# Kernel optimization log

Measured on AMD Instinct MI355X. Metric: run time of the kernel, lower is better.

## Reference

```python
import jax, jax.numpy as jnp
from jax import lax
import numpy as np

B, C, H, W = 4, 128, 160, 160
C2 = 2 * C          # dwconv / channel-attention width
FP_HID = 2 * C      # Feature_Pool ratio=2
CA_HID = C2 // 16   # Channel_Attention ratio=16


def setup_inputs() -> dict:
    key = jax.random.key(0)
    ks = jax.random.split(key, 20)
    s = lambda *sh: 0.02
    return {
        "RGB": jax.random.normal(ks[0], (B, C, H, W), jnp.float32),
        "T": jax.random.normal(ks[1], (B, C, H, W), jnp.float32),
        # Feature_Pool (shared module applied to both RGB and T)
        "fp_down_w": jax.random.normal(ks[2], (FP_HID, C), jnp.float32) * 0.02,
        "fp_down_b": jnp.zeros((FP_HID,), jnp.float32),
        "fp_up_w": jax.random.normal(ks[3], (C, FP_HID), jnp.float32) * 0.02,
        "fp_up_b": jnp.zeros((C,), jnp.float32),
        # dwconv: Conv2d(2c, 2c, k=7, pad=3, groups=c) -> weight [2c, 2, 7, 7]
        "dw_w": jax.random.normal(ks[4], (C2, 2, 7, 7), jnp.float32) * 0.02,
        "dw_b": jnp.zeros((C2,), jnp.float32),
        # Channel_Attention on 2c
        "ca_down_w": jax.random.normal(ks[5], (CA_HID, C2), jnp.float32) * 0.02,
        "ca_down_b": jnp.zeros((CA_HID,), jnp.float32),
        "ca_up_w": jax.random.normal(ks[6], (C2, CA_HID), jnp.float32) * 0.02,
        "ca_up_b": jnp.zeros((C2,), jnp.float32),
        # Spatial_Attention 1x1 convs (c -> 1), stored as [c] vectors + scalar bias
        "sr_w": jax.random.normal(ks[7], (C,), jnp.float32) * 0.02,
        "sr_b": jnp.zeros((1,), jnp.float32),
        "st_w": jax.random.normal(ks[8], (C,), jnp.float32) * 0.02,
        "st_b": jnp.zeros((1,), jnp.float32),
    }


def _feature_pool(x, dw, db, uw, ub):
    # AdaptiveAvgPool2d(1) -> Linear -> GELU(exact) -> Linear ; returns [b, c]
    y = jnp.mean(x, axis=(2, 3))
    y = jax.nn.gelu(y @ dw.T + db, approximate=False)
    return y @ uw.T + ub


def _channel_att(x, dw, db, uw, ub):
    # AdaptiveMaxPool2d(1) -> Linear -> GELU(exact) -> Linear ; returns [b, 2c, 1, 1]
    y = jnp.max(x, axis=(2, 3))
    y = jax.nn.gelu(y @ dw.T + db, approximate=False)
    y = y @ uw.T + ub
    return y[:, :, None, None]


def reference(RGB, T, fp_down_w, fp_down_b, fp_up_w, fp_up_b, dw_w, dw_b,
              ca_down_w, ca_down_b, ca_up_w, ca_up_b, sr_w, sr_b, st_w, st_b):
    b, c, h, w = RGB.shape
    rgb_y = _feature_pool(RGB, fp_down_w, fp_down_b, fp_up_w, fp_up_b)
    t_y = _feature_pool(T, fp_down_w, fp_down_b, fp_up_w, fp_up_b)
    rgb_y = rgb_y / jnp.linalg.norm(rgb_y, axis=1, keepdims=True)
    t_y = t_y / jnp.linalg.norm(t_y, axis=1, keepdims=True)
    # logits_per = c * rgb_y[b,c,1] @ t_y[b,1,c] -> [b, c, c]
    logits = c * rgb_y[:, :, None] * t_y[:, None, :]
    # Faithful to torch.diagonal default (dim1=0, dim2=1): result[j,k] = logits[k,k,j],
    # shape [c, min(b,c)] = [c, b]; then reshape to (b, c, 1, 1). Requires b <= c.
    diag = jnp.diagonal(logits, axis1=0, axis2=1)
    cross_gate = jax.nn.sigmoid(diag).reshape(b, c, 1, 1)
    add_gate = 1.0 - cross_gate

    New_RGB_e = RGB * cross_gate
    New_T_e = T * cross_gate
    New_RGB_c = RGB * add_gate
    New_T_c = T * add_gate

    x_cat_e = jnp.concatenate([New_RGB_e, New_T_e], axis=1)  # [b, 2c, h, w]
    dw_out = lax.conv_general_dilated(
        x_cat_e, dw_w, window_strides=(1, 1), padding=[(3, 3), (3, 3)],
        dimension_numbers=("NCHW", "OIHW", "NCHW"), feature_group_count=c,
    ) + dw_b[None, :, None, None]

    fuse_gate = jax.nn.sigmoid(_channel_att(dw_out, ca_down_w, ca_down_b, ca_up_w, ca_up_b))
    rgb_gate_e, t_gate_e = fuse_gate[:, :c], fuse_gate[:, c:]

    New_RGB = New_RGB_e * rgb_gate_e + New_RGB_c
    New_T = New_T_e * t_gate_e + New_T_c

    # 1x1 conv c->1 (with bias) for each stream
    f_r = jnp.einsum("bchw,c->bhw", New_RGB, sr_w)[:, None] + sr_b[0]  # [b,1,h,w]
    f_t = jnp.einsum("bchw,c->bhw", New_T, st_w)[:, None] + st_b[0]
    att = jax.nn.softmax(jnp.concatenate([f_r, f_t], axis=1), axis=1)  # [b,2,h,w]

    New_RGB = New_RGB * att[:, 0:1]
    New_T = New_T * att[:, 1:2]
    return New_RGB, New_T
```

## Files before the change

kernel.cpp:

```cpp
#include <hip/hip_runtime.h>
#include <cfloat>
#include <cmath>

#define HW 25600
#define WIDTH 160
#define NB 4
#define NC 128

typedef float f32x2 __attribute__((ext_vector_type(2)));
typedef _Float16 h2 __attribute__((ext_vector_type(2)));

__device__ __forceinline__ float gelu_exact(float x) {
    return 0.5f * x * (1.f + erff(x * 0.70710678118654752f));
}
__device__ __forceinline__ float sigmoidf_(float x) {
    return 1.f / (1.f + expf(-x));
}

__device__ __forceinline__ unsigned pack_pkrtz(float a, float b) {
    return __builtin_bit_cast(unsigned, __builtin_amdgcn_cvt_pkrtz(a, b));
}
__device__ __forceinline__ h2 u2h(unsigned u) {
    return __builtin_bit_cast(h2, u);
}
__device__ __forceinline__ float h2sum(h2 h) {
    return (float)h[0] + (float)h[1];
}
__device__ __forceinline__ h2 fma2h(h2 a, h2 b, h2 c) {
    return __builtin_elementwise_fma(a, b, c);
}

__global__ __launch_bounds__(256) void mean_pack_kernel(const float* __restrict__ RGB,
                                                        const float* __restrict__ T,
                                                        const float* __restrict__ dww,
                                                        float* __restrict__ means,
                                                        unsigned* __restrict__ wpk) {
    int p = blockIdx.x;
    if (p >= 1024) {
        int i = (p - 1024) * 256 + threadIdx.x;
        if (i < 128 * 98) {
            int g = i / 98; int r = i - g * 98;
            int ky = r / 14; int r2 = r - ky * 14;
            int oc = r2 / 7; int kx = r2 - oc * 7;
            int o = 2 * g + oc;
            float wa = dww[(o * 2 + 0) * 49 + ky * 7 + kx];
            float wb = dww[(o * 2 + 1) * 49 + ky * 7 + kx];
            wpk[i] = pack_pkrtz(wa, wb);
        }
        return;
    }
    const float* src = (p < 512) ? (RGB + (size_t)p * HW)
                                 : (T + (size_t)(p - 512) * HW);
    const float4* s4 = (const float4*)src;
    float s = 0.f;
    for (int i = threadIdx.x; i < HW / 4; i += 256) {
        float4 v = s4[i];
        s += (v.x + v.y) + (v.z + v.w);
    }
    for (int off = 32; off; off >>= 1) s += __shfl_down(s, off);
    __shared__ float r[4];
    if ((threadIdx.x & 63) == 0) r[threadIdx.x >> 6] = s;
    __syncthreads();
    if (threadIdx.x == 0) means[p] = (r[0] + r[1] + r[2] + r[3]) * (1.f / (float)HW);
}

__global__ __launch_bounds__(256) void mlp_kernel(const float* __restrict__ means,
                                                  const float* __restrict__ dww,
                                                  const float* __restrict__ dwb,
                                                  const float* __restrict__ uww,
                                                  const float* __restrict__ uwb,
                                                  float* __restrict__ ynorm) {
    int tb = blockIdx.x;
    int t = threadIdx.x;
    __shared__ float sm[128];
    __shared__ float sh[256];
    __shared__ float zz[256];
    __shared__ float r4[4];
    if (t < 128) sm[t] = means[tb * 128 + t];
    __syncthreads();
    float a = dwb[t];
    const float* wrow = dww + t * 128;
    for (int c = 0; c < 128; ++c) a += wrow[c] * sm[c];
    sh[t] = gelu_exact(a);
    __syncthreads();
    int c = t & 127, half = t >> 7;
    float z = 0.f;
    const float* urow = uww + c * 256 + half * 128;
    const float* hh = sh + half * 128;
    for (int j = 0; j < 128; ++j) z += urow[j] * hh[j];
    zz[t] = z;
    __syncthreads();
    float y = 0.f;
    if (t < 128) y = zz[t] + zz[t + 128] + uwb[t];
    float p = y * y;
    for (int off = 32; off; off >>= 1) p += __shfl_down(p, off);
    if ((t & 63) == 0) r4[t >> 6] = p;
    __syncthreads();
    float nrm = sqrtf(r4[0] + r4[1] + r4[2] + r4[3]);
    if (t < 128) ynorm[tb * 128 + t] = y / nrm;
}

#define TW2 166
#define THR 22
#define NYT 10
__global__ __launch_bounds__(256, 4) void conv_max_kernel(const float* __restrict__ RGB,
                                                          const float* __restrict__ T,
                                                          const unsigned* __restrict__ wpk,
                                                          const float* __restrict__ ynorm,
                                                          float* __restrict__ part) {
    int orig = blockIdx.x;
    int wg = (orig & 7) * 640 + (orig >> 3);
    int b  = wg / 1280;
    int rr = wg - b * 1280;
    int g  = rr / NYT;
    int yt = rr - g * NYT;
    int t  = threadIdx.x;
    __shared__ unsigned tile[THR * TW2];
    __shared__ float r0s[4], r1s[4];
    int ic0 = 2 * g;
    int c0 = ic0 & 127, c1 = (ic0 + 1) & 127;
    const float* base = (ic0 < 128) ? RGB : T;
    const float* plane0 = base + ((size_t)(b * 128 + c0)) * HW;
    const float* plane1 = base + ((size_t)(b * 128 + c1)) * HW;
    int i0 = b * 128 + c0, i1 = b * 128 + c1;
    int j0 = i0 & 3, k0 = i0 >> 2, j1 = i1 & 3, k1 = i1 >> 2;
    float gate0 = sigmoidf_(128.f * ynorm[j0 * 128 + j0] * ynorm[512 + j0 * 128 + k0]);
    float gate1 = sigmoidf_(128.f * ynorm[j1 * 128 + j1] * ynorm[512 + j1 * 128 + k1]);
    int y0 = yt * 16 - 3;
    for (int e = t; e < THR * TW2; e += 256) {
        int row = e / TW2;
        int col = e - row * TW2;
        int gy = y0 + row, gx = col - 3;
        float v0 = 0.f, v1 = 0.f;
        if (gy >= 0 && gy < 160 && gx >= 0 && gx < 160) {
            int off = gy * WIDTH + gx;
            v0 = plane0[off] * gate0;
            v1 = plane1[off] * gate1;
        }
        tile[e] = pack_pkrtz(v0, v1);
    }
    __syncthreads();
    int xs = (t & 15) * 10;
    int ys = t >> 4;
    h2 zz = (h2)0;
    h2 A0 = zz, A1 = zz, A2 = zz, A3 = zz, A4 = zz;
    h2 A5 = zz, A6 = zz, A7 = zz, A8 = zz, A9 = zz;
    h2 B0 = zz, B1 = zz, B2 = zz, B3 = zz, B4 = zz;
    h2 B5 = zz, B6 = zz, B7 = zz, B8 = zz, B9 = zz;
    const unsigned* wgp = wpk + g * 98;
    #pragma unroll
    for (int ky = 0; ky < 7; ++ky) {
        unsigned wk[14];
        #pragma unroll
        for (int j = 0; j < 14; ++j) wk[j] = wgp[ky * 14 + j];
        const uint2* tr2 = (const uint2*)(tile + (ys + ky) * TW2 + xs);
        unsigned win[16];
        #pragma unroll
        for (int j = 0; j < 8; ++j) {
            uint2 p = tr2[j];
            win[2 * j] = p.x;
            win[2 * j + 1] = p.y;
        }
        #pragma unroll
        for (int kx = 0; kx < 7; ++kx) {
            h2 w0 = u2h(wk[kx]);
            h2 w1 = u2h(wk[7 + kx]);
            h2 v;
            v = u2h(win[kx + 0]); A0 = fma2h(w0, v, A0); B0 = fma2h(w1, v, B0);
            v = u2h(win[kx + 1]); A1 = fma2h(w0, v, A1); B1 = fma2h(w1, v, B1);
            v = u2h(win[kx + 2]); A2 = fma2h(w0, v, A2); B2 = fma2h(w1, v, B2);
            v = u2h(win[kx + 3]); A3 = fma2h(w0, v, A3); B3 = fma2h(w1, v, B3);
            v = u2h(win[kx + 4]); A4 = fma2h(w0, v, A4); B4 = fma2h(w1, v, B4);
            v = u2h(win[kx + 5]); A5 = fma2h(w0, v, A5); B5 = fma2h(w1, v, B5);
            v = u2h(win[kx + 6]); A6 = fma2h(w0, v, A6); B6 = fma2h(w1, v, B6);
            v = u2h(win[kx + 7]); A7 = fma2h(w0, v, A7); B7 = fma2h(w1, v, B7);
            v = u2h(win[kx + 8]); A8 = fma2h(w0, v, A8); B8 = fma2h(w1, v, B8);
            v = u2h(win[kx + 9]); A9 = fma2h(w0, v, A9); B9 = fma2h(w1, v, B9);
        }
    }
    float m0 = fmaxf(fmaxf(fmaxf(h2sum(A0), h2sum(A1)), fmaxf(h2sum(A2), h2sum(A3))),
                     fmaxf(fmaxf(h2sum(A4), h2sum(A5)),
                           fmaxf(fmaxf(h2sum(A6), h2sum(A7)), fmaxf(h2sum(A8), h2sum(A9)))));
    float m1 = fmaxf(fmaxf(fmaxf(h2sum(B0), h2sum(B1)), fmaxf(h2sum(B2), h2sum(B3))),
                     fmaxf(fmaxf(h2sum(B4), h2sum(B5)),
                           fmaxf(fmaxf(h2sum(B6), h2sum(B7)), fmaxf(h2sum(B8), h2sum(B9)))));
    for (int off = 32; off; off >>= 1) {
        m0 = fmaxf(m0, __shfl_down(m0, off));
        m1 = fmaxf(m1, __shfl_down(m1, off));
    }
    if ((t & 63) == 0) { r0s[t >> 6] = m0; r1s[t >> 6] = m1; }
    __syncthreads();
    if (t == 0) {
        m0 = fmaxf(fmaxf(r0s[0], r0s[1]), fmaxf(r0s[2], r0s[3]));
        m1 = fmaxf(fmaxf(r1s[0], r1s[1]), fmaxf(r1s[2], r1s[3]));
        int bb = ((b * 128 + g) * NYT + yt) * 2;
        part[bb] = m0;
        part[bb + 1] = m1;
    }
}

__global__ __launch_bounds__(256) void att_kernel(const float* __restrict__ ynorm,
                                                  const float* __restrict__ part,
                                                  const float* __restrict__ dwb,
                                                  const float* __restrict__ cdw,
                                                  const float* __restrict__ cdb,
                                                  const float* __restrict__ cuw,
                                                  const float* __restrict__ cub,
                                                  const float* __restrict__ srw,
                                                  const float* __restrict__ stw,
                                                  float* __restrict__ coefs) {
    int t = threadIdx.x;
    __shared__ float scg[512];
    __shared__ float smax[1024];
    __shared__ float sh2[64];
    __shared__ float sfg[1024];
    for (int idx = t; idx < 512; idx += 256) {
        int kk = idx >> 2, j = idx & 3;
        scg[idx] = sigmoidf_(128.f * ynorm[j * 128 + j] * ynorm[512 + j * 128 + kk]);
    }
    for (int idx = t; idx < 1024; idx += 256) {
        int b = idx >> 8, o = idx & 255;
        int gg = o >> 1, oc = o & 1;
        const float* pp = part + ((b * 128 + gg) * NYT) * 2 + oc;
        float m = pp[0];
        #pragma unroll
        for (int yt = 1; yt < NYT; ++yt) m = fmaxf(m, pp[yt * 2]);
        smax[idx] = m + dwb[o];
    }
    __syncthreads();
    if (t < 64) {
        int b = t >> 4, j = t & 15;
        float a = cdb[j];
        const float* wrow = cdw + j * 256;
        const float* mx = smax + b * 256;
        for (int o = 0; o < 256; ++o) a += wrow[o] * mx[o];
        sh2[t] = gelu_exact(a);
    }
    __syncthreads();
    for (int idx = t; idx < 1024; idx += 256) {
        int b = idx >> 8, o = idx & 255;
        float z = cub[o];
        const float* ur = cuw + o * 16;
        const float* hh = sh2 + b * 16;
        #pragma unroll
        for (int j = 0; j < 16; ++j) z += ur[j] * hh[j];
        sfg[idx] = sigmoidf_(z);
    }
    __syncthreads();
    for (int idx = t; idx < 512; idx += 256) {
        int b = idx >> 7, c = idx & 127;
        float cgv = scg[idx];
        float ar = cgv * sfg[b * 256 + c] + 1.f - cgv;
        float at = cgv * sfg[b * 256 + 128 + c] + 1.f - cgv;
        coefs[idx] = ar;
        coefs[512 + idx] = at;
        coefs[1024 + idx] = ar * srw[c];
        coefs[1536 + idx] = at * stw[c];
    }
}

__global__ __launch_bounds__(512, 4) void fuse_kernel(const float* __restrict__ RGB,
                                                      const float* __restrict__ T,
                                                      const float* __restrict__ coefs,
                                                      const float* __restrict__ srb,
                                                      const float* __restrict__ stb,
                                                      float* __restrict__ out) {
    int b = blockIdx.y;
    int t = threadIdx.x;
    int w = t >> 6, lane = t & 63;
    int pix = blockIdx.x * 128 + lane * 2;
    __shared__ float sco[4][128];
    if (t < 512) {
        int a = t >> 7, c = t & 127;
        sco[a][c] = coefs[a * 512 + b * 128 + c];
    }
    __syncthreads();
    const float* rp = RGB + (size_t)b * NC * HW;
    const float* tp = T + (size_t)b * NC * HW;
    f32x2 rv[16], tv[16];
    f32x2 df; df.x = 0.f; df.y = 0.f;
    #pragma unroll
    for (int ci = 0; ci < 16; ++ci) {
        int c = w * 16 + ci;
        size_t off = (size_t)c * HW + pix;
        rv[ci] = *(const f32x2*)(rp + off);
        tv[ci] = *(const f32x2*)(tp + off);
        float wrc = sco[2][c], wtc = sco[3][c];
        df.x += rv[ci].x * wrc - tv[ci].x * wtc;
        df.y += rv[ci].y * wrc - tv[ci].y * wtc;
    }
    __shared__ f32x2 sdf[8][64];
    sdf[w][lane] = df;
    __syncthreads();
    float sx = srb[0] - stb[0], sy = sx;
    #pragma unroll
    for (int ww = 0; ww < 8; ++ww) {
        f32x2 d = sdf[ww][lane];
        sx += d.x;
        sy += d.y;
    }
    float ax = sigmoidf_(sx), ay = sigmoidf_(sy);
    float* outR = out + (size_t)b * NC * HW;
    float* outT = out + (size_t)NB * NC * HW + (size_t)b * NC * HW;
    #pragma unroll
    for (int ci = 0; ci < 16; ++ci) {
        int c = w * 16 + ci;
        size_t off = (size_t)c * HW + pix;
        float arc = sco[0][c], atc = sco[1][c];
        f32x2 o1, o2;
        o1.x = rv[ci].x * arc * ax;         o1.y = rv[ci].y * arc * ay;
        o2.x = tv[ci].x * atc * (1.f - ax); o2.y = tv[ci].y * atc * (1.f - ay);
        __builtin_nontemporal_store(o1, (f32x2*)(outR + off));
        __builtin_nontemporal_store(o2, (f32x2*)(outT + off));
    }
}

extern "C" void kernel_launch(void* const* d_in, const int* in_sizes, int n_in,
                              void* d_out, int out_size, void* d_ws, size_t ws_size,
                              hipStream_t stream) {
    const float* RGB       = (const float*)d_in[0];
    const float* T         = (const float*)d_in[1];
    const float* fp_down_w = (const float*)d_in[2];
    const float* fp_down_b = (const float*)d_in[3];
    const float* fp_up_w   = (const float*)d_in[4];
    const float* fp_up_b   = (const float*)d_in[5];
    const float* dw_w      = (const float*)d_in[6];
    const float* dw_b      = (const float*)d_in[7];
    const float* ca_down_w = (const float*)d_in[8];
    const float* ca_down_b = (const float*)d_in[9];
    const float* ca_up_w   = (const float*)d_in[10];
    const float* ca_up_b   = (const float*)d_in[11];
    const float* sr_w      = (const float*)d_in[12];
    const float* sr_b      = (const float*)d_in[13];
    const float* st_w      = (const float*)d_in[14];
    const float* st_b      = (const float*)d_in[15];
    float* out = (float*)d_out;
    float* ws  = (float*)d_ws;

    unsigned* wpk = (unsigned*)(ws + 14336);
    mean_pack_kernel<<<1073, 256, 0, stream>>>(RGB, T, dw_w, ws, wpk);
    mlp_kernel<<<8, 256, 0, stream>>>(ws, fp_down_w, fp_down_b, fp_up_w, fp_up_b, ws + 1024);
    conv_max_kernel<<<5120, 256, 0, stream>>>(RGB, T, wpk, ws + 1024, ws + 2048);
    att_kernel<<<1, 256, 0, stream>>>(ws + 1024, ws + 2048, dw_b, ca_down_w, ca_down_b,
                                      ca_up_w, ca_up_b, sr_w, st_w, ws + 12288);
    fuse_kernel<<<dim3(200, 4), 512, 0, stream>>>(RGB, T, ws + 12288, sr_b, st_b, out);
}
```

Measured before the change: 134.0 us.

## Fuse channel-attention MLP into fuse kernel and simplify tile-load indexing

Removes the single-block att_kernel launch and has every fuse block redundantly compute the channel-attention MLP and gate coefficients for its batch, with the down-projection split across 256 threads. This eliminates one launch, its serial tail, and the coefs round-trip through global memory. The cost is 800 blocks each redoing the small reduction over part and the MLP before streaming. The conv tile loader also replaces per-element division with incremental row/col stepping and unsigned bounds checks.

```diff
diff --git a/kernel.cpp b/kernel.cpp
--- a/kernel.cpp
+++ b/kernel.cpp
@@ -127,26 +127,31 @@
     float gate0 = sigmoidf_(128.f * ynorm[j0 * 128 + j0] * ynorm[512 + j0 * 128 + k0]);
     float gate1 = sigmoidf_(128.f * ynorm[j1 * 128 + j1] * ynorm[512 + j1 * 128 + k1]);
     int y0 = yt * 16 - 3;
-    for (int e = t; e < THR * TW2; e += 256) {
-        int row = e / TW2;
-        int col = e - row * TW2;
-        int gy = y0 + row, gx = col - 3;
-        float v0 = 0.f, v1 = 0.f;
-        if (gy >= 0 && gy < 160 && gx >= 0 && gx < 160) {
-            int off = gy * WIDTH + gx;
-            v0 = plane0[off] * gate0;
-            v1 = plane1[off] * gate1;
+    {
+        int row = t / TW2;
+        int col = t - row * TW2;
+        for (int e = t; e < THR * TW2; e += 256) {
+            int gy = y0 + row, gx = col - 3;
+            float v0 = 0.f, v1 = 0.f;
+            if ((unsigned)gy < 160u && (unsigned)gx < 160u) {
+                int off = gy * WIDTH + gx;
+                v0 = plane0[off] * gate0;
+                v1 = plane1[off] * gate1;
+            }
+            tile[e] = pack_pkrtz(v0, v1);
+            col += 256 - TW2;
+            ++row;
+            if (col >= TW2) { col -= TW2; ++row; }
         }
-        tile[e] = pack_pkrtz(v0, v1);
     }
     __syncthreads();
     int xs = (t & 15) * 10;
     int ys = t >> 4;
-    h2 zz = (h2)0;
-    h2 A0 = zz, A1 = zz, A2 = zz, A3 = zz, A4 = zz;
-    h2 A5 = zz, A6 = zz, A7 = zz, A8 = zz, A9 = zz;
-    h2 B0 = zz, B1 = zz, B2 = zz, B3 = zz, B4 = zz;
-    h2 B5 = zz, B6 = zz, B7 = zz, B8 = zz, B9 = zz;
+    h2 zzv = (h2)0;
+    h2 A0 = zzv, A1 = zzv, A2 = zzv, A3 = zzv, A4 = zzv;
+    h2 A5 = zzv, A6 = zzv, A7 = zzv, A8 = zzv, A9 = zzv;
+    h2 B0 = zzv, B1 = zzv, B2 = zzv, B3 = zzv, B4 = zzv;
+    h2 B5 = zzv, B6 = zzv, B7 = zzv, B8 = zzv, B9 = zzv;
     const unsigned* wgp = wpk + g * 98;
     #pragma unroll
     for (int ky = 0; ky < 7; ++ky) {
@@ -199,80 +204,75 @@
     }
 }
 
-__global__ __launch_bounds__(256) void att_kernel(const float* __restrict__ ynorm,
-                                                  const float* __restrict__ part,
-                                                  const float* __restrict__ dwb,
-                                                  const float* __restrict__ cdw,
-                                                  const float* __restrict__ cdb,
-                                                  const float* __restrict__ cuw,
-                                                  const float* __restrict__ cub,
-                                                  const float* __restrict__ srw,
-                                                  const float* __restrict__ stw,
-                                                  float* __restrict__ coefs) {
-    int t = threadIdx.x;
-    __shared__ float scg[512];
-    __shared__ float smax[1024];
-    __shared__ float sh2[64];
-    __shared__ float sfg[1024];
-    for (int idx = t; idx < 512; idx += 256) {
-        int kk = idx >> 2, j = idx & 3;
-        scg[idx] = sigmoidf_(128.f * ynorm[j * 128 + j] * ynorm[512 + j * 128 + kk]);
-    }
-    for (int idx = t; idx < 1024; idx += 256) {
-        int b = idx >> 8, o = idx & 255;
-        int gg = o >> 1, oc = o & 1;
-        const float* pp = part + ((b * 128 + gg) * NYT) * 2 + oc;
-        float m = pp[0];
-        #pragma unroll
-        for (int yt = 1; yt < NYT; ++yt) m = fmaxf(m, pp[yt * 2]);
-        smax[idx] = m + dwb[o];
-    }
-    __syncthreads();
-    if (t < 64) {
-        int b = t >> 4, j = t & 15;
-        float a = cdb[j];
-        const float* wrow = cdw + j * 256;
-        const float* mx = smax + b * 256;
-        for (int o = 0; o < 256; ++o) a += wrow[o] * mx[o];
-        sh2[t] = gelu_exact(a);
-    }
-    __syncthreads();
-    for (int idx = t; idx < 1024; idx += 256) {
-        int b = idx >> 8, o = idx & 255;
-        float z = cub[o];
-        const float* ur = cuw + o * 16;
-        const float* hh = sh2 + b * 16;
-        #pragma unroll
-        for (int j = 0; j < 16; ++j) z += ur[j] * hh[j];
-        sfg[idx] = sigmoidf_(z);
-    }
-    __syncthreads();
-    for (int idx = t; idx < 512; idx += 256) {
-        int b = idx >> 7, c = idx & 127;
-        float cgv = scg[idx];
-        float ar = cgv * sfg[b * 256 + c] + 1.f - cgv;
-        float at = cgv * sfg[b * 256 + 128 + c] + 1.f - cgv;
-        coefs[idx] = ar;
-        coefs[512 + idx] = at;
-        coefs[1024 + idx] = ar * srw[c];
-        coefs[1536 + idx] = at * stw[c];
-    }
-}
-
-__global__ __launch_bounds__(512, 4) void fuse_kernel(const float* __restrict__ RGB,
-                                                      const float* __restrict__ T,
-                                                      const float* __restrict__ coefs,
-                                                      const float* __restrict__ srb,
-                                                      const float* __restrict__ stb,
-                                                      float* __restrict__ out) {
+__global__ __launch_bounds__(512, 4) void fuse_att_kernel(const float* __restrict__ RGB,
+                                                          const float* __restrict__ T,
+                                                          const float* __restrict__ part,
+                                                          const float* __restrict__ ynorm,
+                                                          const float* __restrict__ dwb,
+                                                          const float* __restrict__ cdw,
+                                                          const float* __restrict__ cdb,
+                                                          const float* __restrict__ cuw,
+                                                          const float* __restrict__ cub,
+                                                          const float* __restrict__ srw,
+                                                          const float* __restrict__ stw,
+                                                          const float* __restrict__ srb,
+                                                          const float* __restrict__ stb,
+                                                          float* __restrict__ out) {
     int b = blockIdx.y;
     int t = threadIdx.x;
     int w = t >> 6, lane = t & 63;
     int pix = blockIdx.x * 128 + lane * 2;
+    __shared__ float smax[256];
+    __shared__ float part_d[256];
+    __shared__ float sh2[16];
+    __shared__ float sfg[256];
     __shared__ float sco[4][128];
-    if (t < 512) {
-        int a = t >> 7, c = t & 127;
-        sco[a][c] = coefs[a * 512 + b * 128 + c];
+    if (t < 256) {
+        int o = t, gg = o >> 1, oc = o & 1;
+        const float* pp = part + ((b * 128 + gg) * NYT) * 2 + oc;
+        float m = pp[0];
+        #pragma unroll
+        for (int yt = 1; yt < NYT; ++yt) m = fmaxf(m, pp[yt * 2]);
+        smax[o] = m + dwb[o];
+    }
+    __syncthreads();
+    if (t < 256) {
+        int j = t & 15, seg = t >> 4;
+        const float* wrow = cdw + j * 256 + seg * 16;
+        const float* mx = smax + seg * 16;
+        float a = 0.f;
+        #pragma unroll
+        for (int o = 0; o < 16; ++o) a += wrow[o] * mx[o];
+        part_d[t] = a;
+    }
+    __syncthreads();
+    if (t < 16) {
+        float a = cdb[t];
+        #pragma unroll
+        for (int s = 0; s < 16; ++s) a += part_d[s * 16 + t];
+        sh2[t] = gelu_exact(a);
+    }
+    __syncthreads();
+    if (t < 256) {
+        int o = t;
+        float z = cub[o];
+        const float* ur = cuw + o * 16;
+        #pragma unroll
+        for (int j = 0; j < 16; ++j) z += ur[j] * sh2[j];
+        sfg[o] = sigmoidf_(z);
+    }
+    __syncthreads();
+    if (t < 128) {
+        int c = t;
+        int idx = b * 128 + c;
+        int kk = idx >> 2, j2 = idx & 3;
+        float cg = sigmoidf_(128.f * ynorm[j2 * 128 + j2] * ynorm[512 + j2 * 128 + kk]);
+        float ar = cg * sfg[c] + 1.f - cg;
+        float at = cg * sfg[128 + c] + 1.f - cg;
+        sco[0][c] = ar;
+        sco[1][c] = at;
+        sco[2][c] = ar * srw[c];
+        sco[3][c] = at * stw[c];
     }
     __syncthreads();
     const float* rp = RGB + (size_t)b * NC * HW;
@@ -341,7 +341,8 @@
     mean_pack_kernel<<<1073, 256, 0, stream>>>(RGB, T, dw_w, ws, wpk);
     mlp_kernel<<<8, 256, 0, stream>>>(ws, fp_down_w, fp_down_b, fp_up_w, fp_up_b, ws + 1024);
     conv_max_kernel<<<5120, 256, 0, stream>>>(RGB, T, wpk, ws + 1024, ws + 2048);
-    att_kernel<<<1, 256, 0, stream>>>(ws + 1024, ws + 2048, dw_b, ca_down_w, ca_down_b,
-                                      ca_up_w, ca_up_b, sr_w, st_w, ws + 12288);
-    fuse_kernel<<<dim3(200, 4), 512, 0, stream>>>(RGB, T, ws + 12288, sr_b, st_b, out);
-}
+    fuse_att_kernel<<<dim3(200, 4), 512, 0, stream>>>(RGB, T, ws + 2048, ws + 1024,
+                                                      dw_b, ca_down_w, ca_down_b,
+                                                      ca_up_w, ca_up_b, sr_w, st_w,
+                                                      sr_b, st_b, out);
+}
```

After: 127.9 us. -4.6%, faster.
